# Optimization experiments

Hardware: AMD Instinct MI355X
Metric: run time of the kernel (lower is better)

## Reference

```python
import jax, jax.numpy as jnp
import numpy as np


def _bilerp(grid, x, y):
    """Bilinear sample grid [H,W,C] at continuous coords x,y [B,V] -> [B,V,C]."""
    H, W = grid.shape[0], grid.shape[1]
    x0f = jnp.floor(x); y0f = jnp.floor(y)
    wx = (x - x0f)[..., None]; wy = (y - y0f)[..., None]
    x0 = jnp.clip(x0f.astype(jnp.int32), 0, W - 1)
    x1 = jnp.clip(x0f.astype(jnp.int32) + 1, 0, W - 1)
    y0 = jnp.clip(y0f.astype(jnp.int32), 0, H - 1)
    y1 = jnp.clip(y0f.astype(jnp.int32) + 1, 0, H - 1)
    return (grid[y0, x0] * (1 - wx) * (1 - wy) + grid[y0, x1] * wx * (1 - wy)
            + grid[y1, x0] * (1 - wx) * wy + grid[y1, x1] * wx * wy)


def _normalize(x, eps=1e-12):
    n = jnp.linalg.norm(x, axis=-1, keepdims=True)
    return x / jnp.maximum(n, eps)


def setup_inputs() -> dict:
    key = jax.random.key(0)
    ks = jax.random.split(key, 12)
    B, H, W = 4, 512, 512
    V, F = 100000, 200000
    return {
        "vertices": jax.random.normal(ks[0], (1, V, 3), jnp.float32),
        "vertices_texcoords": jax.random.uniform(ks[1], (1, V, 2), jnp.float32),
        "vertices_normals": jax.random.normal(ks[2], (1, V, 3), jnp.float32),
        "faces_vt_idx": jax.random.randint(ks[3], (1, F, 3), 0, V, jnp.int32),
        "faces_vn_idx": jax.random.randint(ks[4], (1, F, 3), 0, V, jnp.int32),
        "faces_v_idx": jax.random.randint(ks[5], (1, F, 3), 0, V, jnp.int32),
        "pose": jax.random.normal(ks[6], (B, 4, 4), jnp.float32),
        "depth": jax.random.uniform(ks[7], (B, H, W), jnp.float32),
        "face_index_map": jax.random.randint(ks[8], (B, H, W), 0, F, jnp.int32),
        "weight_map": jax.random.uniform(ks[9], (B, H, W, 3), jnp.float32),
        "v_uvz": jax.random.uniform(ks[10], (B, V, 3), jnp.float32),
        # +0.5 keeps the z component (used as 1/z) away from zero
        "faces_v_uvz": jax.random.uniform(ks[11], (B, F, 3, 3), jnp.float32) + 0.5,
    }


def reference(vertices, vertices_texcoords, vertices_normals, faces_vt_idx,
              faces_vn_idx, faces_v_idx, pose, depth, face_index_map,
              weight_map, v_uvz, faces_v_uvz):
    B, H, W = depth.shape
    mesh_span = (vertices[0].max(axis=0) - vertices[0].min(axis=0)).max()

    # --- screen-space vertex coords + bilinear depth lookup (front mask) ---
    vx = (v_uvz[..., 0] * 0.5 + 0.5) * W                  # [B,V]
    vy = (1.0 - (v_uvz[..., 1] * 0.5 + 0.5)) * H          # [B,V]
    v_depth = _bilerp(depth[0][..., None], vx, vy)        # [B,V,1] (batch-0 depth, as in source)
    v_front_mask = (v_uvz[0, :, 2] - v_depth[0, :, 0] < mesh_span * 0.005)[None, :]

    # --- perspective-corrected barycentric weights ---
    fz = faces_v_uvz[..., 2]                              # [B,F,3]
    fz_map = jax.vmap(lambda f, idx: f[idx])(fz, face_index_map)  # [B,H,W,3]
    wmap = (1.0 / fz_map) * weight_map * depth[..., None] # [B,H,W,3]
    wmap = wmap[..., None]                                # [B,H,W,3,1]

    # --- uv map ---
    faces_vt = vertices_texcoords[0][faces_vt_idx[0]]     # [F,3,2]
    uv_map = (faces_vt[face_index_map] * wmap).sum(axis=-2)  # [B,H,W,2]
    uv_map = uv_map - jnp.floor(uv_map)

    # --- normal map (object + camera space) ---
    faces_vn = vertices_normals[0][faces_vn_idx[0]]       # [F,3,3]
    normal_map = _normalize((faces_vn[face_index_map] * wmap).sum(axis=-2))
    R = pose[:, :3, :3]
    t = pose[:, :3, -1]
    normal_map_cam = _normalize(jnp.einsum('bij,bhwj->bhwi', R, normal_map))

    # --- position map (object + camera space) ---
    faces_v = vertices[0][faces_v_idx[0]]                 # [F,3,3]
    position_map = (faces_v[face_index_map] * wmap).sum(axis=-2)
    position_map_cam = jnp.einsum('bij,bhwj->bhwi', R, position_map) + t[:, None, None, :]

    # Concatenate float map outputs into one tensor [B,H,W,14]
    out = jnp.concatenate([uv_map, normal_map, normal_map_cam,
                           position_map, position_map_cam], axis=-1)
    return out
```

## Files before the change

### kernel.cpp

```cpp
#include <hip/hip_runtime.h>
#include <stdint.h>


struct H2 { _Float16 x, y; };
static __device__ __forceinline__ uint32_t packh_u(float a, float b) {
    H2 h; h.x = (_Float16)a; h.y = (_Float16)b;
    return __builtin_bit_cast(uint32_t, h);
}
static __device__ __forceinline__ float packh(float a, float b) {
    return __builtin_bit_cast(float, packh_u(a, b));
}
static __device__ __forceinline__ float asf(uint32_t u) {
    return __builtin_bit_cast(float, u);
}
static __device__ __forceinline__ float2 unph(float w) {
    H2 h = __builtin_bit_cast(H2, w);
    return make_float2((float)h.x, (float)h.y);
}


__global__ __launch_bounds__(256) void prep_fz(
    const float* __restrict__ nrm, const float* __restrict__ vtx,
    const float* __restrict__ fuvz,
    uint2* __restrict__ nrmh, uint2* __restrict__ vtxh,
    float4* __restrict__ fzq, int V, long BF)
{
    __shared__ float sf[2304];
    const int tid = threadIdx.x;
    const long base = (long)blockIdx.x * 256;
    const long i = base + tid;

    if (nrmh != nullptr && i < V) {
        const float* n = nrm + i * 3;
        const float* v = vtx + i * 3;
        nrmh[i] = make_uint2(packh_u(n[0], n[1]), packh_u(n[2], 0.0f));
        vtxh[i] = make_uint2(packh_u(v[0], v[1]), packh_u(v[2], 0.0f));
    }

    if (base + 256 <= BF) {
        const float4* src = (const float4*)(fuvz + base * 9);
        float4* d = (float4*)sf;
        d[tid]       = src[tid];
        d[tid + 256] = src[tid + 256];
        if (tid < 64) d[tid + 512] = src[tid + 512];
        __syncthreads();
        fzq[i] = make_float4(__fdiv_rn(1.0f, sf[tid * 9 + 2]),
                             __fdiv_rn(1.0f, sf[tid * 9 + 5]),
                             __fdiv_rn(1.0f, sf[tid * 9 + 8]), 0.0f);
    } else if (i < BF) {
        const float* s = fuvz + i * 9;
        fzq[i] = make_float4(__fdiv_rn(1.0f, s[2]),
                             __fdiv_rn(1.0f, s[5]),
                             __fdiv_rn(1.0f, s[8]), 0.0f);
    }
}

__global__ __launch_bounds__(256) void pack_faces2(
    const float* __restrict__ tc,
    const uint2* __restrict__ nrmh, const uint2* __restrict__ vtxh,
    const int* __restrict__ f_vt, const int* __restrict__ f_vn,
    const int* __restrict__ f_v,
    float4* __restrict__ rec, int F, int V)
{
    __shared__ float4 sw[1024];
    const int tid  = threadIdx.x;
    const int base = blockIdx.x * 256;
    const int f    = base + tid;

    if (f < F) {
        float2 t[3]; uint2 N[3], Vv[3];
#pragma unroll
        for (int k = 0; k < 3; ++k) {
            int ivt = f_vt[f * 3 + k];
            ivt = ivt < 0 ? 0 : (ivt >= V ? V - 1 : ivt);
            t[k] = ((const float2*)tc)[ivt];
            int ivn = f_vn[f * 3 + k];
            ivn = ivn < 0 ? 0 : (ivn >= V ? V - 1 : ivn);
            N[k] = nrmh[ivn];
            int iv = f_v[f * 3 + k];
            iv = iv < 0 ? 0 : (iv >= V ? V - 1 : iv);
            Vv[k] = vtxh[iv];
        }
        uint32_t w9  = (N[0].y  & 0xffffu) | (N[1].y  << 16);
        uint32_t w10 = (N[2].y  & 0xffffu) | (Vv[0].y << 16);
        uint32_t w14 = (Vv[1].y & 0xffffu) | (Vv[2].y << 16);
        float4* o = sw + tid * 4;
        o[0] = make_float4(t[0].x, t[0].y, t[1].x, t[1].y);
        o[1] = make_float4(t[2].x, t[2].y, asf(N[0].x), asf(N[1].x));
        o[2] = make_float4(asf(N[2].x), asf(w9), asf(w10), asf(Vv[0].x));
        o[3] = make_float4(asf(Vv[1].x), asf(Vv[2].x), asf(w14), 0.0f);
    }
    __syncthreads();
    const int valid  = F - base;
    const int valid4 = (valid < 256 ? valid : 256) * 4;
    float4* og = rec + (long)base * 4;
#pragma unroll
    for (int j = 0; j < 4; ++j) {
        int k = tid + 256 * j;
        if (k < valid4) og[k] = sw[k];
    }
}

__global__ __launch_bounds__(256) void pack_faces_old(
    const float* __restrict__ tc, const float* __restrict__ nrm,
    const float* __restrict__ vtx,
    const int* __restrict__ f_vt, const int* __restrict__ f_vn,
    const int* __restrict__ f_v,
    float* __restrict__ rec, int F, int V)
{
    int f = blockIdx.x * 256 + threadIdx.x;
    if (f >= F) return;
    float t[6], n[9], v[9];
#pragma unroll
    for (int k = 0; k < 3; ++k) {
        int ivt = f_vt[f * 3 + k];
        ivt = ivt < 0 ? 0 : (ivt >= V ? V - 1 : ivt);
        t[k * 2 + 0] = tc[(long)ivt * 2 + 0];
        t[k * 2 + 1] = tc[(long)ivt * 2 + 1];
        int ivn = f_vn[f * 3 + k];
        ivn = ivn < 0 ? 0 : (ivn >= V ? V - 1 : ivn);
        n[k * 3 + 0] = nrm[(long)ivn * 3 + 0];
        n[k * 3 + 1] = nrm[(long)ivn * 3 + 1];
        n[k * 3 + 2] = nrm[(long)ivn * 3 + 2];
        int iv = f_v[f * 3 + k];
        iv = iv < 0 ? 0 : (iv >= V ? V - 1 : iv);
        v[k * 3 + 0] = vtx[(long)iv * 3 + 0];
        v[k * 3 + 1] = vtx[(long)iv * 3 + 1];
        v[k * 3 + 2] = vtx[(long)iv * 3 + 2];
    }
    float4* o = (float4*)(rec + (long)f * 16);
    o[0] = make_float4(t[0], t[1], t[2], t[3]);
    o[1] = make_float4(t[4], t[5], packh(n[0], n[1]), packh(n[3], n[4]));
    o[2] = make_float4(packh(n[6], n[7]), packh(n[2], n[5]),
                       packh(n[8], v[2]), packh(v[0], v[1]));
    o[3] = make_float4(packh(v[3], v[4]), packh(v[6], v[7]),
                       packh(v[5], v[8]), 0.0f);
}

__global__ __launch_bounds__(256) void raster_fast4(
    const float4* __restrict__ rec,
    const float4* __restrict__ fzq,
    const float* __restrict__ pose,
    const float* __restrict__ depth,
    const int*   __restrict__ fim,
    const float* __restrict__ weight,
    float* __restrict__ out,
    int F, int HW, int nx, int swz)
{
    __shared__ float4 st[1024];
    __shared__ float  sb[256 * 14];
    const int tid  = threadIdx.x;
    const int lane = tid & 63;
    const int wav  = tid >> 6;
    const int id   = blockIdx.x;
    int b, x;
    if (swz) {
        const int xcd = id & 7;
        b = xcd >> 1;
        x = (id >> 3) + ((xcd & 1) ? (nx >> 1) : 0);
    } else {
        b = id / nx;
        x = id - b * nx;
    }
    const int hw  = x * 256 + tid;
    const long p  = (long)b * HW + hw;

    const float* pb = pose + b * 16;
    float R00 = pb[0],  R01 = pb[1],  R02 = pb[2],  t0 = pb[3];
    float R10 = pb[4],  R11 = pb[5],  R12 = pb[6],  t1 = pb[7];
    float R20 = pb[8],  R21 = pb[9],  R22 = pb[10], t2 = pb[11];

    int f = fim[p];
    f = f < 0 ? 0 : (f >= F ? F - 1 : f);
    const float d = depth[p];
    float w0 = weight[p * 3 + 0];
    float w1 = weight[p * 3 + 1];
    float w2 = weight[p * 3 + 2];

    float4 fz = fzq[(long)b * F + f];

    {
        const int pc = lane & 3;
        float4 v[4]; int rw[4];
#pragma unroll
        for (int j = 0; j < 4; ++j) {
            rw[j] = (lane >> 2) + 16 * j;
            int fr = __shfl(f, rw[j], 64);
            v[j] = rec[(long)fr * 4 + pc];
        }
#pragma unroll
        for (int j = 0; j < 4; ++j) {
            st[wav * 256 + rw[j] * 4 + (pc ^ ((rw[j] >> 1) & 3))] = v[j];
        }
    }
    asm volatile("s_waitcnt lgkmcnt(0)" ::: "memory");
    __builtin_amdgcn_sched_barrier(0);

    const int rbase = wav * 256 + lane * 4;
    const int rs    = (lane >> 1) & 3;
    float4 a0 = st[rbase + (0 ^ rs)];
    float4 a1 = st[rbase + (1 ^ rs)];
    float4 a2 = st[rbase + (2 ^ rs)];
    float4 a3 = st[rbase + (3 ^ rs)];

    float wm0 = __fmul_rn(__fmul_rn(fz.x, w0), d);
    float wm1 = __fmul_rn(__fmul_rn(fz.y, w1), d);
    float wm2 = __fmul_rn(__fmul_rn(fz.z, w2), d);

    float uv0 = __fadd_rn(__fadd_rn(__fmul_rn(a0.x, wm0), __fmul_rn(a0.z, wm1)),
                          __fmul_rn(a1.x, wm2));
    float uv1 = __fadd_rn(__fadd_rn(__fmul_rn(a0.y, wm0), __fmul_rn(a0.w, wm1)),
                          __fmul_rn(a1.y, wm2));
    uv0 -= floorf(uv0);
    uv1 -= floorf(uv1);

    float2 u6  = unph(a1.z);
    float2 u7  = unph(a1.w);
    float2 u8  = unph(a2.x);
    float2 u9  = unph(a2.y);
    float2 u10 = unph(a2.z);
    float2 u11 = unph(a2.w);
    float2 u12 = unph(a3.x);
    float2 u13 = unph(a3.y);
    float2 u14 = unph(a3.z);

    float n0 = u6.x * wm0 + u7.x * wm1 + u8.x * wm2;
    float n1 = u6.y * wm0 + u7.y * wm1 + u8.y * wm2;
    float n2 = u9.x * wm0 + u9.y * wm1 + u10.x * wm2;

    float p0 = u11.x * wm0 + u12.x * wm1 + u13.x * wm2;
    float p1 = u11.y * wm0 + u12.y * wm1 + u13.y * wm2;
    float p2 = u10.y * wm0 + u14.x * wm1 + u14.y * wm2;

    float nn = sqrtf(n0 * n0 + n1 * n1 + n2 * n2);
    float ni = 1.0f / fmaxf(nn, 1e-12f);
    float m0 = n0 * ni, m1 = n1 * ni, m2 = n2 * ni;

    float c0 = R00 * m0 + R01 * m1 + R02 * m2;
    float c1 = R10 * m0 + R11 * m1 + R12 * m2;
    float c2 = R20 * m0 + R21 * m1 + R22 * m2;
    float cn = sqrtf(c0 * c0 + c1 * c1 + c2 * c2);
    float ci = 1.0f / fmaxf(cn, 1e-12f);
    c0 *= ci; c1 *= ci; c2 *= ci;

    float q0 = R00 * p0 + R01 * p1 + R02 * p2 + t0;
    float q1 = R10 * p0 + R11 * p1 + R12 * p2 + t1;
    float q2 = R20 * p0 + R21 * p1 + R22 * p2 + t2;

    float* s = sb + tid * 14;
    s[0]  = uv0; s[1]  = uv1;
    s[2]  = m0;  s[3]  = m1;  s[4]  = m2;
    s[5]  = c0;  s[6]  = c1;  s[7]  = c2;
    s[8]  = p0;  s[9]  = p1;  s[10] = p2;
    s[11] = q0;  s[12] = q1;  s[13] = q2;
    __syncthreads();

    float4* og = (float4*)(out + ((long)b * HW + (long)x * 256) * 14);
    const float4* sv = (const float4*)sb;
#pragma unroll
    for (int j = 0; j < 4; ++j) {
        int k = tid + 256 * j;
        if (k < 896) og[k] = sv[k];
    }
}

__global__ __launch_bounds__(256) void raster_fast3(
    const float4* __restrict__ rec, const float4* __restrict__ fzq,
    const float* __restrict__ pose, const float* __restrict__ depth,
    const int*   __restrict__ fim, const float* __restrict__ weight,
    float* __restrict__ out, int F, int HW, int nx, int swz)
{
    __shared__ float sb[256 * 14];
    const int tid = threadIdx.x;
    const int id  = blockIdx.x;
    int b, x;
    if (swz) {
        const int xcd = id & 7;
        b = xcd >> 1;
        x = (id >> 3) + ((xcd & 1) ? (nx >> 1) : 0);
    } else {
        b = id / nx;
        x = id - b * nx;
    }
    const int hw  = x * 256 + tid;
    const long p  = (long)b * HW + hw;
    const float* pb = pose + b * 16;
    float R00 = pb[0],  R01 = pb[1],  R02 = pb[2],  t0 = pb[3];
    float R10 = pb[4],  R11 = pb[5],  R12 = pb[6],  t1 = pb[7];
    float R20 = pb[8],  R21 = pb[9],  R22 = pb[10], t2 = pb[11];
    int f = fim[p];
    f = f < 0 ? 0 : (f >= F ? F - 1 : f);
    const float d = depth[p];
    float w0 = weight[p * 3 + 0];
    float w1 = weight[p * 3 + 1];
    float w2 = weight[p * 3 + 2];
    const float4* R4 = rec + (long)f * 4;
    float4 a0 = R4[0], a1 = R4[1], a2 = R4[2], a3 = R4[3];
    float4 fz = fzq[(long)b * F + f];
    float wm0 = __fmul_rn(__fmul_rn(fz.x, w0), d);
    float wm1 = __fmul_rn(__fmul_rn(fz.y, w1), d);
    float wm2 = __fmul_rn(__fmul_rn(fz.z, w2), d);
    float uv0 = __fadd_rn(__fadd_rn(__fmul_rn(a0.x, wm0), __fmul_rn(a0.z, wm1)),
                          __fmul_rn(a1.x, wm2));
    float uv1 = __fadd_rn(__fadd_rn(__fmul_rn(a0.y, wm0), __fmul_rn(a0.w, wm1)),
                          __fmul_rn(a1.y, wm2));
    uv0 -= floorf(uv0);
    uv1 -= floorf(uv1);
    float2 u6  = unph(a1.z), u7  = unph(a1.w), u8  = unph(a2.x);
    float2 u9  = unph(a2.y), u10 = unph(a2.z), u11 = unph(a2.w);
    float2 u12 = unph(a3.x), u13 = unph(a3.y), u14 = unph(a3.z);
    float n0 = u6.x * wm0 + u7.x * wm1 + u8.x * wm2;
    float n1 = u6.y * wm0 + u7.y * wm1 + u8.y * wm2;
    float n2 = u9.x * wm0 + u9.y * wm1 + u10.x * wm2;
    float p0 = u11.x * wm0 + u12.x * wm1 + u13.x * wm2;
    float p1 = u11.y * wm0 + u12.y * wm1 + u13.y * wm2;
    float p2 = u10.y * wm0 + u14.x * wm1 + u14.y * wm2;
    float nn = sqrtf(n0 * n0 + n1 * n1 + n2 * n2);
    float ni = 1.0f / fmaxf(nn, 1e-12f);
    float m0 = n0 * ni, m1 = n1 * ni, m2 = n2 * ni;
    float c0 = R00 * m0 + R01 * m1 + R02 * m2;
    float c1 = R10 * m0 + R11 * m1 + R12 * m2;
    float c2 = R20 * m0 + R21 * m1 + R22 * m2;
    float cn = sqrtf(c0 * c0 + c1 * c1 + c2 * c2);
    float ci = 1.0f / fmaxf(cn, 1e-12f);
    c0 *= ci; c1 *= ci; c2 *= ci;
    float q0 = R00 * p0 + R01 * p1 + R02 * p2 + t0;
    float q1 = R10 * p0 + R11 * p1 + R12 * p2 + t1;
    float q2 = R20 * p0 + R21 * p1 + R22 * p2 + t2;
    float* s = sb + tid * 14;
    s[0]  = uv0; s[1]  = uv1;
    s[2]  = m0;  s[3]  = m1;  s[4]  = m2;
    s[5]  = c0;  s[6]  = c1;  s[7]  = c2;
    s[8]  = p0;  s[9]  = p1;  s[10] = p2;
    s[11] = q0;  s[12] = q1;  s[13] = q2;
    __syncthreads();
    float4* og = (float4*)(out + ((long)b * HW + (long)x * 256) * 14);
    const float4* sv = (const float4*)sb;
#pragma unroll
    for (int j = 0; j < 4; ++j) {
        int k = tid + 256 * j;
        if (k < 896) og[k] = sv[k];
    }
}

__global__ __launch_bounds__(256) void raster_kernel(
    const float* __restrict__ vertices, const float* __restrict__ texcoords,
    const float* __restrict__ normals,
    const int* __restrict__ f_vt, const int* __restrict__ f_vn,
    const int* __restrict__ f_v,
    const float* __restrict__ pose, const float* __restrict__ depth,
    const int* __restrict__ fim, const float* __restrict__ weight,
    const float* __restrict__ fuvz, float* __restrict__ out, int F, int V,
    int HW)
{
    const int hw = blockIdx.x * 256 + threadIdx.x;
    if (hw >= HW) return;
    const int b  = blockIdx.y;
    const int p  = b * HW + hw;
    const float* pb = pose + b * 16;
    float R00 = pb[0], R01 = pb[1], R02 = pb[2],  t0 = pb[3];
    float R10 = pb[4], R11 = pb[5], R12 = pb[6],  t1 = pb[7];
    float R20 = pb[8], R21 = pb[9], R22 = pb[10], t2 = pb[11];
    int f = fim[p];
    f = f < 0 ? 0 : (f >= F ? F - 1 : f);
    const float d = depth[p];
    const float* fz = fuvz + ((long)b * F + f) * 9;
    float wm[3];
#pragma unroll
    for (int k = 0; k < 3; ++k)
        wm[k] = __fmul_rn(__fmul_rn(__fdiv_rn(1.0f, fz[k * 3 + 2]),
                                    weight[(long)p * 3 + k]), d);
    float u0t[3], u1t[3];
    float n0 = 0.f, n1 = 0.f, n2 = 0.f, p0 = 0.f, p1 = 0.f, p2 = 0.f;
#pragma unroll
    for (int k = 0; k < 3; ++k) {
        int ivt = f_vt[f * 3 + k], ivn = f_vn[f * 3 + k], iv = f_v[f * 3 + k];
        ivt = ivt < 0 ? 0 : (ivt >= V ? V - 1 : ivt);
        ivn = ivn < 0 ? 0 : (ivn >= V ? V - 1 : ivn);
        iv  = iv  < 0 ? 0 : (iv  >= V ? V - 1 : iv);
        const float* tc = texcoords + (long)ivt * 2;
        u0t[k] = __fmul_rn(tc[0], wm[k]);
        u1t[k] = __fmul_rn(tc[1], wm[k]);
        const float* nr = normals + (long)ivn * 3;
        n0 += nr[0] * wm[k]; n1 += nr[1] * wm[k]; n2 += nr[2] * wm[k];
        const float* vv = vertices + (long)iv * 3;
        p0 += vv[0] * wm[k]; p1 += vv[1] * wm[k]; p2 += vv[2] * wm[k];
    }
    float uv0 = __fadd_rn(__fadd_rn(u0t[0], u0t[1]), u0t[2]);
    float uv1 = __fadd_rn(__fadd_rn(u1t[0], u1t[1]), u1t[2]);
    uv0 -= floorf(uv0); uv1 -= floorf(uv1);
    float nn = sqrtf(n0 * n0 + n1 * n1 + n2 * n2);
    float ni = 1.0f / fmaxf(nn, 1e-12f);
    float m0 = n0 * ni, m1 = n1 * ni, m2 = n2 * ni;
    float c0 = R00 * m0 + R01 * m1 + R02 * m2;
    float c1 = R10 * m0 + R11 * m1 + R12 * m2;
    float c2 = R20 * m0 + R21 * m1 + R22 * m2;
    float cn = sqrtf(c0 * c0 + c1 * c1 + c2 * c2);
    float ci = 1.0f / fmaxf(cn, 1e-12f);
    c0 *= ci; c1 *= ci; c2 *= ci;
    float q0 = R00 * p0 + R01 * p1 + R02 * p2 + t0;
    float q1 = R10 * p0 + R11 * p1 + R12 * p2 + t1;
    float q2 = R20 * p0 + R21 * p1 + R22 * p2 + t2;
    float2* o = (float2*)(out + (long)p * 14);
    o[0] = make_float2(uv0, uv1); o[1] = make_float2(m0, m1);
    o[2] = make_float2(m2, c0);   o[3] = make_float2(c1, c2);
    o[4] = make_float2(p0, p1);   o[5] = make_float2(p2, q0);
    o[6] = make_float2(q1, q2);
}

extern "C" void kernel_launch(void* const* d_in, const int* in_sizes, int n_in,
                              void* d_out, int out_size, void* d_ws, size_t ws_size,
                              hipStream_t stream) {
    const float* vertices  = (const float*)d_in[0];
    const float* texcoords = (const float*)d_in[1];
    const float* normals   = (const float*)d_in[2];
    const int*   f_vt      = (const int*)  d_in[3];
    const int*   f_vn      = (const int*)  d_in[4];
    const int*   f_v       = (const int*)  d_in[5];
    const float* pose      = (const float*)d_in[6];
    const float* depth     = (const float*)d_in[7];
    const int*   fim       = (const int*)  d_in[8];
    const float* weight    = (const float*)d_in[9];
    const float* fuvz      = (const float*)d_in[11];
    float* out = (float*)d_out;

    const int B  = in_sizes[6] / 16;
    const int F  = in_sizes[3] / 3;
    const int V  = in_sizes[1] / 2;
    const int HW = in_sizes[7] / B;
    const long BF = (long)B * F;

    const size_t rec_bytes = (size_t)F * 64;
    const size_t fzq_bytes = (size_t)BF * 16;
    const size_t tab_bytes = (size_t)V * 8;
    const bool base_ok = d_ws != nullptr &&
                         (((uintptr_t)d_ws) & 127) == 0 &&
                         (HW % 256) == 0;
    const bool ws_new = base_ok &&
                        ws_size >= rec_bytes + fzq_bytes + 2 * tab_bytes;
    const bool ws_old = base_ok && ws_size >= rec_bytes + fzq_bytes;

    const int nx = HW / 256;
    const int swz = (B == 4 && (nx & 1) == 0) ? 1 : 0;

    if (ws_new) {
        float* rec  = (float*)d_ws;
        float* fzq  = (float*)((char*)d_ws + rec_bytes);
        uint2* nrmh = (uint2*)((char*)d_ws + rec_bytes + fzq_bytes);
        uint2* vtxh = (uint2*)((char*)d_ws + rec_bytes + fzq_bytes + tab_bytes);
        long nb = BF > (long)V ? BF : (long)V;
        prep_fz<<<(unsigned)((nb + 255) / 256), 256, 0, stream>>>(
            normals, vertices, fuvz, nrmh, vtxh, (float4*)fzq, V, BF);
        pack_faces2<<<(F + 255) / 256, 256, 0, stream>>>(
            texcoords, nrmh, vtxh, f_vt, f_vn, f_v, (float4*)rec, F, V);
        raster_fast4<<<B * nx, 256, 0, stream>>>(
            (const float4*)rec, (const float4*)fzq, pose, depth, fim, weight,
            out, F, HW, nx, swz);
    } else if (ws_old) {
        float* rec = (float*)d_ws;
        float* fzq = (float*)((char*)d_ws + rec_bytes);
        prep_fz<<<(unsigned)((BF + 255) / 256), 256, 0, stream>>>(
            normals, vertices, fuvz, nullptr, nullptr, (float4*)fzq, V, BF);
        pack_faces_old<<<(F + 255) / 256, 256, 0, stream>>>(
            texcoords, normals, vertices, f_vt, f_vn, f_v, rec, F, V);
        raster_fast3<<<B * nx, 256, 0, stream>>>(
            (const float4*)rec, (const float4*)fzq, pose, depth, fim, weight,
            out, F, HW, nx, swz);
    } else {
        dim3 grid((HW + 255) / 256, B);
        raster_kernel<<<grid, 256, 0, stream>>>(
            vertices, texcoords, normals, f_vt, f_vn, f_v,
            pose, depth, fim, weight, fuvz, out, F, V, HW);
    }
}
```

Before: 175.7 us.

## Fold per-batch inverse z into 128-byte face records for single-gather rasterization

Precomputed 1/z values for all four batches are now stored inside each face record, which grows from 64 to 128 bytes. The separate fzq array and its extra gather go away. The fz computation moves from prep_fz into the face-packing kernel, and prep_fz is reduced to a vertex-table kernel. The raster kernel now reads each face record directly, dropping the shuffle/LDS-swizzle gather, so one 128-byte line serves both geometry and depth factors. In exchange, the packing writes more bytes and the path is restricted to B==4.

```diff
diff --git a/kernel.cpp b/kernel.cpp
--- a/kernel.cpp
+++ b/kernel.cpp
@@ -18,6 +18,207 @@
     return make_float2((float)h.x, (float)h.y);
 }
 
+
+__global__ __launch_bounds__(256) void prep_tab(
+    const float* __restrict__ nrm, const float* __restrict__ vtx,
+    uint2* __restrict__ nrmh, uint2* __restrict__ vtxh, int V)
+{
+    int i = blockIdx.x * 256 + threadIdx.x;
+    if (i >= V) return;
+    const float* n = nrm + (long)i * 3;
+    const float* v = vtx + (long)i * 3;
+    nrmh[i] = make_uint2(packh_u(n[0], n[1]), packh_u(n[2], 0.0f));
+    vtxh[i] = make_uint2(packh_u(v[0], v[1]), packh_u(v[2], 0.0f));
+}
+
+__global__ __launch_bounds__(256) void pack_faces3(
+    const float* __restrict__ tc,
+    const uint2* __restrict__ nrmh, const uint2* __restrict__ vtxh,
+    const int* __restrict__ f_vt, const int* __restrict__ f_vn,
+    const int* __restrict__ f_v, const float* __restrict__ fuvz,
+    float4* __restrict__ rec, int F, int V)
+{
+    __shared__ float4 sw[2048];
+    float* sf = (float*)sw;
+    const int tid  = threadIdx.x;
+    const int base = blockIdx.x * 256;
+    const int f    = base + tid;
+    const bool full = (base + 256 <= F) && ((((long)F * 9) & 3) == 0);
+
+    float2 t[3]; uint2 N[3], Vv[3];
+    if (f < F) {
+#pragma unroll
+        for (int k = 0; k < 3; ++k) {
+            int ivt = f_vt[f * 3 + k];
+            ivt = ivt < 0 ? 0 : (ivt >= V ? V - 1 : ivt);
+            t[k] = ((const float2*)tc)[ivt];
+            int ivn = f_vn[f * 3 + k];
+            ivn = ivn < 0 ? 0 : (ivn >= V ? V - 1 : ivn);
+            N[k] = nrmh[ivn];
+            int iv = f_v[f * 3 + k];
+            iv = iv < 0 ? 0 : (iv >= V ? V - 1 : iv);
+            Vv[k] = vtxh[iv];
+        }
+    }
+
+    float fzr[4][3];
+    if (full) {
+#pragma unroll 1
+        for (int b = 0; b < 4; ++b) {
+            const float4* src = (const float4*)(fuvz + ((long)b * F + base) * 9);
+            __syncthreads();
+            sw[tid]       = src[tid];
+            sw[tid + 256] = src[tid + 256];
+            if (tid < 64) sw[tid + 512] = src[tid + 512];
+            __syncthreads();
+            fzr[b][0] = __fdiv_rn(1.0f, sf[tid * 9 + 2]);
+            fzr[b][1] = __fdiv_rn(1.0f, sf[tid * 9 + 5]);
+            fzr[b][2] = __fdiv_rn(1.0f, sf[tid * 9 + 8]);
+        }
+    } else if (f < F) {
+#pragma unroll
+        for (int b = 0; b < 4; ++b) {
+            const float* s = fuvz + ((long)b * F + f) * 9;
+            fzr[b][0] = __fdiv_rn(1.0f, s[2]);
+            fzr[b][1] = __fdiv_rn(1.0f, s[5]);
+            fzr[b][2] = __fdiv_rn(1.0f, s[8]);
+        }
+    }
+
+    uint32_t w9 = 0, w10 = 0, w14 = 0;
+    if (f < F) {
+        w9  = (N[0].y  & 0xffffu) | (N[1].y  << 16);
+        w10 = (N[2].y  & 0xffffu) | (Vv[0].y << 16);
+        w14 = (Vv[1].y & 0xffffu) | (Vv[2].y << 16);
+    }
+    __syncthreads();
+
+    if (full) {
+        float4* o = sw + tid * 8;
+        o[0] = make_float4(t[0].x, t[0].y, t[1].x, t[1].y);
+        o[1] = make_float4(t[2].x, t[2].y, asf(N[0].x), asf(N[1].x));
+        o[2] = make_float4(asf(N[2].x), asf(w9), asf(w10), asf(Vv[0].x));
+        o[3] = make_float4(asf(Vv[1].x), asf(Vv[2].x), asf(w14), 0.0f);
+#pragma unroll
+        for (int b = 0; b < 4; ++b)
+            o[4 + b] = make_float4(fzr[b][0], fzr[b][1], fzr[b][2], 0.0f);
+        __syncthreads();
+        float4* og = rec + (long)base * 8;
+#pragma unroll
+        for (int j = 0; j < 8; ++j)
+            og[tid + 256 * j] = sw[tid + 256 * j];
+    } else if (f < F) {
+        float4* o = rec + (long)f * 8;
+        o[0] = make_float4(t[0].x, t[0].y, t[1].x, t[1].y);
+        o[1] = make_float4(t[2].x, t[2].y, asf(N[0].x), asf(N[1].x));
+        o[2] = make_float4(asf(N[2].x), asf(w9), asf(w10), asf(Vv[0].x));
+        o[3] = make_float4(asf(Vv[1].x), asf(Vv[2].x), asf(w14), 0.0f);
+#pragma unroll
+        for (int b = 0; b < 4; ++b)
+            o[4 + b] = make_float4(fzr[b][0], fzr[b][1], fzr[b][2], 0.0f);
+    }
+}
+
+__global__ __launch_bounds__(256) void raster_fast5(
+    const float4* __restrict__ rec,
+    const float* __restrict__ pose,
+    const float* __restrict__ depth,
+    const int*   __restrict__ fim,
+    const float* __restrict__ weight,
+    float* __restrict__ out,
+    int F, int HW, int nx, int swz)
+{
+    __shared__ float sb[256 * 14];
+    const int tid = threadIdx.x;
+    const int id  = blockIdx.x;
+    int b, x;
+    if (swz) {
+        const int xcd = id & 7;
+        b = xcd >> 1;
+        x = (id >> 3) + ((xcd & 1) ? (nx >> 1) : 0);
+    } else {
+        b = id / nx;
+        x = id - b * nx;
+    }
+    const int hw  = x * 256 + tid;
+    const long p  = (long)b * HW + hw;
+
+    const float* pb = pose + b * 16;
+    float R00 = pb[0],  R01 = pb[1],  R02 = pb[2],  t0 = pb[3];
+    float R10 = pb[4],  R11 = pb[5],  R12 = pb[6],  t1 = pb[7];
+    float R20 = pb[8],  R21 = pb[9],  R22 = pb[10], t2 = pb[11];
+
+    int f = fim[p];
+    f = f < 0 ? 0 : (f >= F ? F - 1 : f);
+    const float d = depth[p];
+    float w0 = weight[p * 3 + 0];
+    float w1 = weight[p * 3 + 1];
+    float w2 = weight[p * 3 + 2];
+
+    const float4* R = rec + (long)f * 8;
+    float4 a0 = R[0], a1 = R[1], a2 = R[2], a3 = R[3];
+    float4 fz = R[4 + b];
+
+    float wm0 = __fmul_rn(__fmul_rn(fz.x, w0), d);
+    float wm1 = __fmul_rn(__fmul_rn(fz.y, w1), d);
+    float wm2 = __fmul_rn(__fmul_rn(fz.z, w2), d);
+
+    float uv0 = __fadd_rn(__fadd_rn(__fmul_rn(a0.x, wm0), __fmul_rn(a0.z, wm1)),
+                          __fmul_rn(a1.x, wm2));
+    float uv1 = __fadd_rn(__fadd_rn(__fmul_rn(a0.y, wm0), __fmul_rn(a0.w, wm1)),
+                          __fmul_rn(a1.y, wm2));
+    uv0 -= floorf(uv0);
+    uv1 -= floorf(uv1);
+
+    float2 u6  = unph(a1.z);
+    float2 u7  = unph(a1.w);
+    float2 u8  = unph(a2.x);
+    float2 u9  = unph(a2.y);
+    float2 u10 = unph(a2.z);
+    float2 u11 = unph(a2.w);
+    float2 u12 = unph(a3.x);
+    float2 u13 = unph(a3.y);
+    float2 u14 = unph(a3.z);
+
+    float n0 = u6.x * wm0 + u7.x * wm1 + u8.x * wm2;
+    float n1 = u6.y * wm0 + u7.y * wm1 + u8.y * wm2;
+    float n2 = u9.x * wm0 + u9.y * wm1 + u10.x * wm2;
+
+    float p0 = u11.x * wm0 + u12.x * wm1 + u13.x * wm2;
+    float p1 = u11.y * wm0 + u12.y * wm1 + u13.y * wm2;
+    float p2 = u10.y * wm0 + u14.x * wm1 + u14.y * wm2;
+
+    float nn = sqrtf(n0 * n0 + n1 * n1 + n2 * n2);
+    float ni = 1.0f / fmaxf(nn, 1e-12f);
+    float m0 = n0 * ni, m1 = n1 * ni, m2 = n2 * ni;
+
+    float c0 = R00 * m0 + R01 * m1 + R02 * m2;
+    float c1 = R10 * m0 + R11 * m1 + R12 * m2;
+    float c2 = R20 * m0 + R21 * m1 + R22 * m2;
+    float cn = sqrtf(c0 * c0 + c1 * c1 + c2 * c2);
+    float ci = 1.0f / fmaxf(cn, 1e-12f);
+    c0 *= ci; c1 *= ci; c2 *= ci;
+
+    float q0 = R00 * p0 + R01 * p1 + R02 * p2 + t0;
+    float q1 = R10 * p0 + R11 * p1 + R12 * p2 + t1;
+    float q2 = R20 * p0 + R21 * p1 + R22 * p2 + t2;
+
+    float* s = sb + tid * 14;
+    s[0]  = uv0; s[1]  = uv1;
+    s[2]  = m0;  s[3]  = m1;  s[4]  = m2;
+    s[5]  = c0;  s[6]  = c1;  s[7]  = c2;
+    s[8]  = p0;  s[9]  = p1;  s[10] = p2;
+    s[11] = q0;  s[12] = q1;  s[13] = q2;
+    __syncthreads();
+
+    float4* og = (float4*)(out + ((long)b * HW + (long)x * 256) * 14);
+    const float4* sv = (const float4*)sb;
+#pragma unroll
+    for (int j = 0; j < 4; ++j) {
+        int k = tid + 256 * j;
+        if (k < 896) og[k] = sv[k];
+    }
+}
 
 __global__ __launch_bounds__(256) void prep_fz(
     const float* __restrict__ nrm, const float* __restrict__ vtx,
@@ -55,52 +256,6 @@
     }
 }
 
-__global__ __launch_bounds__(256) void pack_faces2(
-    const float* __restrict__ tc,
-    const uint2* __restrict__ nrmh, const uint2* __restrict__ vtxh,
-    const int* __restrict__ f_vt, const int* __restrict__ f_vn,
-    const int* __restrict__ f_v,
-    float4* __restrict__ rec, int F, int V)
-{
-    __shared__ float4 sw[1024];
-    const int tid  = threadIdx.x;
-    const int base = blockIdx.x * 256;
-    const int f    = base + tid;
-
-    if (f < F) {
-        float2 t[3]; uint2 N[3], Vv[3];
-#pragma unroll
-        for (int k = 0; k < 3; ++k) {
-            int ivt = f_vt[f * 3 + k];
-            ivt = ivt < 0 ? 0 : (ivt >= V ? V - 1 : ivt);
-            t[k] = ((const float2*)tc)[ivt];
-            int ivn = f_vn[f * 3 + k];
-            ivn = ivn < 0 ? 0 : (ivn >= V ? V - 1 : ivn);
-            N[k] = nrmh[ivn];
-            int iv = f_v[f * 3 + k];
-            iv = iv < 0 ? 0 : (iv >= V ? V - 1 : iv);
-            Vv[k] = vtxh[iv];
-        }
-        uint32_t w9  = (N[0].y  & 0xffffu) | (N[1].y  << 16);
-        uint32_t w10 = (N[2].y  & 0xffffu) | (Vv[0].y << 16);
-        uint32_t w14 = (Vv[1].y & 0xffffu) | (Vv[2].y << 16);
-        float4* o = sw + tid * 4;
-        o[0] = make_float4(t[0].x, t[0].y, t[1].x, t[1].y);
-        o[1] = make_float4(t[2].x, t[2].y, asf(N[0].x), asf(N[1].x));
-        o[2] = make_float4(asf(N[2].x), asf(w9), asf(w10), asf(Vv[0].x));
-        o[3] = make_float4(asf(Vv[1].x), asf(Vv[2].x), asf(w14), 0.0f);
-    }
-    __syncthreads();
-    const int valid  = F - base;
-    const int valid4 = (valid < 256 ? valid : 256) * 4;
-    float4* og = rec + (long)base * 4;
-#pragma unroll
-    for (int j = 0; j < 4; ++j) {
-        int k = tid + 256 * j;
-        if (k < valid4) og[k] = sw[k];
-    }
-}
-
 __global__ __launch_bounds__(256) void pack_faces_old(
     const float* __restrict__ tc, const float* __restrict__ nrm,
     const float* __restrict__ vtx,
@@ -135,133 +290,6 @@
                        packh(n[8], v[2]), packh(v[0], v[1]));
     o[3] = make_float4(packh(v[3], v[4]), packh(v[6], v[7]),
                        packh(v[5], v[8]), 0.0f);
-}
-
-__global__ __launch_bounds__(256) void raster_fast4(
-    const float4* __restrict__ rec,
-    const float4* __restrict__ fzq,
-    const float* __restrict__ pose,
-    const float* __restrict__ depth,
-    const int*   __restrict__ fim,
-    const float* __restrict__ weight,
-    float* __restrict__ out,
-    int F, int HW, int nx, int swz)
-{
-    __shared__ float4 st[1024];
-    __shared__ float  sb[256 * 14];
-    const int tid  = threadIdx.x;
-    const int lane = tid & 63;
-    const int wav  = tid >> 6;
-    const int id   = blockIdx.x;
-    int b, x;
-    if (swz) {
-        const int xcd = id & 7;
-        b = xcd >> 1;
-        x = (id >> 3) + ((xcd & 1) ? (nx >> 1) : 0);
-    } else {
-        b = id / nx;
-        x = id - b * nx;
-    }
-    const int hw  = x * 256 + tid;
-    const long p  = (long)b * HW + hw;
-
-    const float* pb = pose + b * 16;
-    float R00 = pb[0],  R01 = pb[1],  R02 = pb[2],  t0 = pb[3];
-    float R10 = pb[4],  R11 = pb[5],  R12 = pb[6],  t1 = pb[7];
-    float R20 = pb[8],  R21 = pb[9],  R22 = pb[10], t2 = pb[11];
-
-    int f = fim[p];
-    f = f < 0 ? 0 : (f >= F ? F - 1 : f);
-    const float d = depth[p];
-    float w0 = weight[p * 3 + 0];
-    float w1 = weight[p * 3 + 1];
-    float w2 = weight[p * 3 + 2];
-
-    float4 fz = fzq[(long)b * F + f];
-
-    {
-        const int pc = lane & 3;
-        float4 v[4]; int rw[4];
-#pragma unroll
-        for (int j = 0; j < 4; ++j) {
-            rw[j] = (lane >> 2) + 16 * j;
-            int fr = __shfl(f, rw[j], 64);
-            v[j] = rec[(long)fr * 4 + pc];
-        }
-#pragma unroll
-        for (int j = 0; j < 4; ++j) {
-            st[wav * 256 + rw[j] * 4 + (pc ^ ((rw[j] >> 1) & 3))] = v[j];
-        }
-    }
-    asm volatile("s_waitcnt lgkmcnt(0)" ::: "memory");
-    __builtin_amdgcn_sched_barrier(0);
-
-    const int rbase = wav * 256 + lane * 4;
-    const int rs    = (lane >> 1) & 3;
-    float4 a0 = st[rbase + (0 ^ rs)];
-    float4 a1 = st[rbase + (1 ^ rs)];
-    float4 a2 = st[rbase + (2 ^ rs)];
-    float4 a3 = st[rbase + (3 ^ rs)];
-
-    float wm0 = __fmul_rn(__fmul_rn(fz.x, w0), d);
-    float wm1 = __fmul_rn(__fmul_rn(fz.y, w1), d);
-    float wm2 = __fmul_rn(__fmul_rn(fz.z, w2), d);
-
-    float uv0 = __fadd_rn(__fadd_rn(__fmul_rn(a0.x, wm0), __fmul_rn(a0.z, wm1)),
-                          __fmul_rn(a1.x, wm2));
-    float uv1 = __fadd_rn(__fadd_rn(__fmul_rn(a0.y, wm0), __fmul_rn(a0.w, wm1)),
-                          __fmul_rn(a1.y, wm2));
-    uv0 -= floorf(uv0);
-    uv1 -= floorf(uv1);
-
-    float2 u6  = unph(a1.z);
-    float2 u7  = unph(a1.w);
-    float2 u8  = unph(a2.x);
-    float2 u9  = unph(a2.y);
-    float2 u10 = unph(a2.z);
-    float2 u11 = unph(a2.w);
-    float2 u12 = unph(a3.x);
-    float2 u13 = unph(a3.y);
-    float2 u14 = unph(a3.z);
-
-    float n0 = u6.x * wm0 + u7.x * wm1 + u8.x * wm2;
-    float n1 = u6.y * wm0 + u7.y * wm1 + u8.y * wm2;
-    float n2 = u9.x * wm0 + u9.y * wm1 + u10.x * wm2;
-
-    float p0 = u11.x * wm0 + u12.x * wm1 + u13.x * wm2;
-    float p1 = u11.y * wm0 + u12.y * wm1 + u13.y * wm2;
-    float p2 = u10.y * wm0 + u14.x * wm1 + u14.y * wm2;
-
-    float nn = sqrtf(n0 * n0 + n1 * n1 + n2 * n2);
-    float ni = 1.0f / fmaxf(nn, 1e-12f);
-    float m0 = n0 * ni, m1 = n1 * ni, m2 = n2 * ni;
-
-    float c0 = R00 * m0 + R01 * m1 + R02 * m2;
-    float c1 = R10 * m0 + R11 * m1 + R12 * m2;
-    float c2 = R20 * m0 + R21 * m1 + R22 * m2;
-    float cn = sqrtf(c0 * c0 + c1 * c1 + c2 * c2);
-    float ci = 1.0f / fmaxf(cn, 1e-12f);
-    c0 *= ci; c1 *= ci; c2 *= ci;
-
-    float q0 = R00 * p0 + R01 * p1 + R02 * p2 + t0;
-    float q1 = R10 * p0 + R11 * p1 + R12 * p2 + t1;
-    float q2 = R20 * p0 + R21 * p1 + R22 * p2 + t2;
-
-    float* s = sb + tid * 14;
-    s[0]  = uv0; s[1]  = uv1;
-    s[2]  = m0;  s[3]  = m1;  s[4]  = m2;
-    s[5]  = c0;  s[6]  = c1;  s[7]  = c2;
-    s[8]  = p0;  s[9]  = p1;  s[10] = p2;
-    s[11] = q0;  s[12] = q1;  s[13] = q2;
-    __syncthreads();
-
-    float4* og = (float4*)(out + ((long)b * HW + (long)x * 256) * 14);
-    const float4* sv = (const float4*)sb;
-#pragma unroll
-    for (int j = 0; j < 4; ++j) {
-        int k = tid + 256 * j;
-        if (k < 896) og[k] = sv[k];
-    }
 }
 
 __global__ __launch_bounds__(256) void raster_fast3(
@@ -430,35 +458,34 @@
     const int HW = in_sizes[7] / B;
     const long BF = (long)B * F;
 
-    const size_t rec_bytes = (size_t)F * 64;
-    const size_t fzq_bytes = (size_t)BF * 16;
-    const size_t tab_bytes = (size_t)V * 8;
+    const size_t rec128_bytes = (size_t)F * 128;
+    const size_t rec64_bytes  = (size_t)F * 64;
+    const size_t fzq_bytes    = (size_t)BF * 16;
+    const size_t tab_bytes    = (size_t)V * 8;
     const bool base_ok = d_ws != nullptr &&
                          (((uintptr_t)d_ws) & 127) == 0 &&
                          (HW % 256) == 0;
-    const bool ws_new = base_ok &&
-                        ws_size >= rec_bytes + fzq_bytes + 2 * tab_bytes;
-    const bool ws_old = base_ok && ws_size >= rec_bytes + fzq_bytes;
+    const bool ws_new = base_ok && B == 4 &&
+                        ws_size >= rec128_bytes + 2 * tab_bytes;
+    const bool ws_old = base_ok && ws_size >= rec64_bytes + fzq_bytes;
 
     const int nx = HW / 256;
     const int swz = (B == 4 && (nx & 1) == 0) ? 1 : 0;
 
     if (ws_new) {
         float* rec  = (float*)d_ws;
-        float* fzq  = (float*)((char*)d_ws + rec_bytes);
-        uint2* nrmh = (uint2*)((char*)d_ws + rec_bytes + fzq_bytes);
-        uint2* vtxh = (uint2*)((char*)d_ws + rec_bytes + fzq_bytes + tab_bytes);
-        long nb = BF > (long)V ? BF : (long)V;
-        prep_fz<<<(unsigned)((nb + 255) / 256), 256, 0, stream>>>(
-            normals, vertices, fuvz, nrmh, vtxh, (float4*)fzq, V, BF);
-        pack_faces2<<<(F + 255) / 256, 256, 0, stream>>>(
-            texcoords, nrmh, vtxh, f_vt, f_vn, f_v, (float4*)rec, F, V);
-        raster_fast4<<<B * nx, 256, 0, stream>>>(
-            (const float4*)rec, (const float4*)fzq, pose, depth, fim, weight,
-            out, F, HW, nx, swz);
+        uint2* nrmh = (uint2*)((char*)d_ws + rec128_bytes);
+        uint2* vtxh = (uint2*)((char*)d_ws + rec128_bytes + tab_bytes);
+        prep_tab<<<(V + 255) / 256, 256, 0, stream>>>(
+            normals, vertices, nrmh, vtxh, V);
+        pack_faces3<<<(F + 255) / 256, 256, 0, stream>>>(
+            texcoords, nrmh, vtxh, f_vt, f_vn, f_v, fuvz,
+            (float4*)rec, F, V);
+        raster_fast5<<<B * nx, 256, 0, stream>>>(
+            (const float4*)rec, pose, depth, fim, weight, out, F, HW, nx, swz);
     } else if (ws_old) {
         float* rec = (float*)d_ws;
-        float* fzq = (float*)((char*)d_ws + rec_bytes);
+        float* fzq = (float*)((char*)d_ws + rec64_bytes);
         prep_fz<<<(unsigned)((BF + 255) / 256), 256, 0, stream>>>(
             normals, vertices, fuvz, nullptr, nullptr, (float4*)fzq, V, BF);
         pack_faces_old<<<(F + 255) / 256, 256, 0, stream>>>(
```

Measured after the change: 182.1 us. 3.7% more time.
